# Kernel optimization log

Measured on AMD Instinct MI355X. Metric: run time of the kernel, lower is better.

## Reference

```python
import jax, jax.numpy as jnp
import numpy as np

B, S, D, E, H = 4, 2048, 1024, 8, 2048


def setup_inputs() -> dict:
    key = jax.random.key(0)
    ks = jax.random.split(key, 8)
    s_in = 1.0 / np.sqrt(D)   # torch Linear default init scale (uniform bound)
    s_hid = 1.0 / np.sqrt(H)
    return {
        "x": jax.random.normal(ks[0], (B, S, D), dtype=jnp.float32),
        "W1": jax.random.uniform(ks[1], (E, D, H), minval=-s_in, maxval=s_in, dtype=jnp.float32),
        "b1": jax.random.uniform(ks[2], (E, H), minval=-s_in, maxval=s_in, dtype=jnp.float32),
        "W2": jax.random.uniform(ks[3], (E, H, D), minval=-s_hid, maxval=s_hid, dtype=jnp.float32),
        "b2": jax.random.uniform(ks[4], (E, D), minval=-s_hid, maxval=s_hid, dtype=jnp.float32),
        "Wg": jax.random.uniform(ks[5], (D, E), minval=-s_in, maxval=s_in, dtype=jnp.float32),
        "bg": jax.random.uniform(ks[6], (E,), minval=-s_in, maxval=s_in, dtype=jnp.float32),
    }


def reference(x, W1, b1, W2, b2, Wg, bg):
    # All-experts dense MoE (eval mode: dropout is identity).
    # hidden: [B,S,E,H]
    h = jax.nn.relu(jnp.einsum("bsd,edh->bseh", x, W1) + b1)
    # expert outputs: [B,S,E,D]
    expert_out = jnp.einsum("bseh,ehd->bsed", h, W2) + b2
    # gate (raw linear, no softmax in original): [B,S,E]
    gate = jnp.einsum("bsd,de->bse", x, Wg) + bg
    # gate-weighted sum over experts -> [B,S,D]
    return jnp.einsum("bse,bsed->bsd", gate, expert_out)
```

## Files before the change

### kernel.cpp

```cpp
#include <hip/hip_runtime.h>

#define NTOK 8192
#define DDIM 1024
#define HDIM 2048
#define NEXP 8
#define GEXP 2

#define BM 256
#define BN 128
#define BK 64

typedef unsigned short u16;
typedef short bf16x8 __attribute__((ext_vector_type(8)));
typedef float f32x4 __attribute__((ext_vector_type(4)));
typedef float float4_t __attribute__((ext_vector_type(4)));

__device__ __forceinline__ u16 f2bf(float f) {
  unsigned u = __float_as_uint(f);
  u += 0x7FFFu + ((u >> 16) & 1u);
  return (u16)(u >> 16);
}

#define GLOAD_LDS16(gp, lp)                                                     \
  __builtin_amdgcn_global_load_lds(                                             \
      (const __attribute__((address_space(1))) unsigned int*)(gp),              \
      (__attribute__((address_space(3))) unsigned int*)(lp), 16, 0, 0)

__global__ void k_prep(const float* __restrict__ x, const float* __restrict__ Wg,
                       const float* __restrict__ bg,
                       u16* __restrict__ xb, float* __restrict__ gate) {
  const int tok = (blockIdx.x * 256 + threadIdx.x) >> 6;
  const int lane = threadIdx.x & 63;
  const float* xr = x + (size_t)tok * DDIM;
  u16* xo = xb + (size_t)tok * DDIM;
  float s[NEXP];
#pragma unroll
  for (int e = 0; e < NEXP; ++e) s[e] = 0.f;
#pragma unroll
  for (int it = 0; it < 2; ++it) {
    const int d0 = lane * 8 + it * 512;
    float4_t v0 = *(const float4_t*)(xr + d0);
    float4_t v1 = *(const float4_t*)(xr + d0 + 4);
    union { bf16x8 v; u16 h[8]; } u;
    u.h[0] = f2bf(v0.x); u.h[1] = f2bf(v0.y); u.h[2] = f2bf(v0.z); u.h[3] = f2bf(v0.w);
    u.h[4] = f2bf(v1.x); u.h[5] = f2bf(v1.y); u.h[6] = f2bf(v1.z); u.h[7] = f2bf(v1.w);
    *(bf16x8*)(xo + d0) = u.v;
    float xv[8] = {v0.x, v0.y, v0.z, v0.w, v1.x, v1.y, v1.z, v1.w};
#pragma unroll
    for (int j = 0; j < 8; ++j) {
      const float4_t w0 = *(const float4_t*)(Wg + (size_t)(d0 + j) * NEXP);
      const float4_t w1 = *(const float4_t*)(Wg + (size_t)(d0 + j) * NEXP + 4);
      s[0] += xv[j] * w0.x; s[1] += xv[j] * w0.y;
      s[2] += xv[j] * w0.z; s[3] += xv[j] * w0.w;
      s[4] += xv[j] * w1.x; s[5] += xv[j] * w1.y;
      s[6] += xv[j] * w1.z; s[7] += xv[j] * w1.w;
    }
  }
#pragma unroll
  for (int off = 32; off; off >>= 1)
#pragma unroll
    for (int e = 0; e < NEXP; ++e) s[e] += __shfl_down(s[e], off);
  if (lane == 0) {
#pragma unroll
    for (int e = 0; e < NEXP; ++e) gate[(size_t)tok * NEXP + e] = s[e] + bg[e];
  }
}

__global__ void k_transpose(const float* __restrict__ in, u16* __restrict__ out,
                            int R, int C, size_t oexp, int orstride) {
  __shared__ float t[64][65];
  const int rb = blockIdx.x * 64, cb = blockIdx.y * 64;
  const float* pin = in + (size_t)blockIdx.z * R * C;
  u16* pout = out + (size_t)blockIdx.z * oexp;
  const int tid = threadIdx.x;
  {
    const int r = tid >> 4;
    const int c4 = (tid & 15) * 4;
#pragma unroll
    for (int i = 0; i < 4; ++i) {
      float4_t v = *(const float4_t*)(pin + (size_t)(rb + r + 16 * i) * C + cb + c4);
      t[r + 16 * i][c4 + 0] = v.x;
      t[r + 16 * i][c4 + 1] = v.y;
      t[r + 16 * i][c4 + 2] = v.z;
      t[r + 16 * i][c4 + 3] = v.w;
    }
  }
  __syncthreads();
  {
    const int oc = tid >> 3;
    const int r8 = (tid & 7) * 8;
#pragma unroll
    for (int jp = 0; jp < 2; ++jp) {
      const int ocol = oc + 32 * jp;
      union { bf16x8 v; u16 h[8]; } u;
#pragma unroll
      for (int k = 0; k < 8; ++k) u.h[k] = f2bf(t[r8 + k][ocol]);
      *(bf16x8*)(pout + (size_t)(cb + ocol) * orstride + rb + r8) = u.v;
    }
  }
}

template <int MODE, int BCH>
__global__ __launch_bounds__(512, 2) void k_gemm(
    const u16* __restrict__ A, int lda,
    const u16* __restrict__ Bt, int ldb,
    const float* __restrict__ bias,
    const float* __restrict__ gate, int ebase,
    void* __restrict__ Cout, int ldc,
    int tilesN, int K, int accum) {
  __shared__ __align__(16) u16 lds[3 * (BM + BN) * BK];
  const int tid = threadIdx.x;
  const int lane = tid & 63;
  const int wid = tid >> 6;
  const int wm = wid >> 1;
  const int wn = wid & 1;

  int nwg = gridDim.x, wg = blockIdx.x;
  int q = nwg >> 3, r8 = nwg & 7;
  int xcd = wg & 7, lo = wg >> 3;
  int swz = (xcd < r8 ? xcd * (q + 1) : r8 * (q + 1) + (xcd - r8) * q) + lo;
  int tm = swz / tilesN, tn = swz % tilesN;
  int bm = tm * BM, bn = tn * BN;

  const int srow = tid >> 3;
  const int scol = ((tid & 7) ^ (srow & 7)) << 3;
  const u16* gA = A + (size_t)(bm + srow) * lda + scol;
  const u16* gB = Bt + (size_t)(bn + srow) * ldb + scol;
  const int dofs = wid * 512;

  u16* a0 = lds;            u16* b0 = lds + BM * BK;
  u16* a1 = b0 + BN * BK;   u16* b1p = a1 + BM * BK;
  u16* a2 = b1p + BN * BK;  u16* b2p = a2 + BM * BK;

#define BOFF(kt) (BCH ? ((size_t)((kt) >> 5) * ((size_t)DDIM * HDIM) +          \
                         (size_t)((kt) & 31) * BK)                              \
                      : (size_t)(kt) * BK)

#define STAGE(aD, bD, kt)                                                       \
  {                                                                             \
    const u16* sa_ = gA + (size_t)(kt) * BK;                                    \
    const u16* sb_ = gB + BOFF(kt);                                             \
    GLOAD_LDS16(sa_,                       (aD) + dofs);                        \
    GLOAD_LDS16(sa_ + (size_t)64 * lda,    (aD) + 4096 + dofs);                 \
    GLOAD_LDS16(sa_ + (size_t)128 * lda,   (aD) + 8192 + dofs);                 \
    GLOAD_LDS16(sa_ + (size_t)192 * lda,   (aD) + 12288 + dofs);                \
    GLOAD_LDS16(sb_,                       (bD) + dofs);                        \
    GLOAD_LDS16(sb_ + (size_t)64 * ldb,    (bD) + 4096 + dofs);                 \
  }

  const int fr = lane & 15;
  const int fq = lane >> 4;
  const int xr = fr & 7;
  const int so0 = ((0 + fq) ^ xr) << 3;
  const int so1 = ((4 + fq) ^ xr) << 3;
  int aro[4], bro[4];
#pragma unroll
  for (int m = 0; m < 4; ++m) aro[m] = (wm * 64 + m * 16 + fr) << 6;
#pragma unroll
  for (int n = 0; n < 4; ++n) bro[n] = (wn * 64 + n * 16 + fr) << 6;

  f32x4 acc[4][4] = {};
  const int nkt = K >> 6;

  STAGE(a0, b0, 0);
  STAGE(a1, b1p, 1);
  asm volatile("s_waitcnt vmcnt(6)" ::: "memory");
  __builtin_amdgcn_s_barrier();
  __builtin_amdgcn_sched_barrier(0);

  u16 *aC = a0, *bC = b0, *aN = a1, *bN = b1p, *aF = a2, *bF = b2p;

#pragma unroll 1
  for (int t = 0; t < nkt; ++t) {
    if (t + 2 < nkt) STAGE(aF, bF, t + 2);
#pragma unroll
    for (int kk = 0; kk < 2; ++kk) {
      const int so = kk ? so1 : so0;
      bf16x8 af[4], bfv[4];
#pragma unroll
      for (int m = 0; m < 4; ++m) af[m] = *(const bf16x8*)(aC + aro[m] + so);
#pragma unroll
      for (int n = 0; n < 4; ++n) bfv[n] = *(const bf16x8*)(bC + bro[n] + so);
      __builtin_amdgcn_s_setprio(1);
#pragma unroll
      for (int m = 0; m < 4; ++m)
#pragma unroll
        for (int n = 0; n < 4; ++n)
          acc[m][n] = __builtin_amdgcn_mfma_f32_16x16x32_bf16(af[m], bfv[n],
                                                              acc[m][n], 0, 0, 0);
      __builtin_amdgcn_s_setprio(0);
    }
    if (t != nkt - 1) {
      if (t + 2 < nkt) {
        asm volatile("s_waitcnt vmcnt(6)" ::: "memory");
      } else {
        asm volatile("s_waitcnt vmcnt(0)" ::: "memory");
      }
      __builtin_amdgcn_s_barrier();
      __builtin_amdgcn_sched_barrier(0);
      u16* tp;
      tp = aC; aC = aN; aN = aF; aF = tp;
      tp = bC; bC = bN; bN = bF; bF = tp;
    }
  }

  const int colbase = bn + wn * 64 + fr;
  if (MODE == 1) {
    const int e = ebase + ((bn + wn * 64) >> 11);
    float bcol[4];
#pragma unroll
    for (int n = 0; n < 4; ++n) bcol[n] = bias[colbase + n * 16];
    u16* O = (u16*)Cout;
#pragma unroll
    for (int m = 0; m < 4; ++m) {
#pragma unroll
      for (int j = 0; j < 4; ++j) {
        int r = bm + wm * 64 + m * 16 + fq * 4 + j;
        float g = gate[(size_t)r * NEXP + e];
#pragma unroll
        for (int n = 0; n < 4; ++n) {
          float v = fmaxf(acc[m][n][j] + bcol[n], 0.f) * g;
          O[(size_t)r * ldc + colbase + n * 16] = f2bf(v);
        }
      }
    }
  } else {
    float* O = (float*)Cout;
    float b2c[4][NEXP];
    if (!accum) {
#pragma unroll
      for (int n = 0; n < 4; ++n)
#pragma unroll
        for (int e = 0; e < NEXP; ++e)
          b2c[n][e] = bias[(size_t)e * DDIM + colbase + n * 16];
    }
#pragma unroll
    for (int m = 0; m < 4; ++m) {
#pragma unroll
      for (int j = 0; j < 4; ++j) {
        int r = bm + wm * 64 + m * 16 + fq * 4 + j;
        if (!accum) {
          float g8[NEXP];
#pragma unroll
          for (int e = 0; e < NEXP; ++e) g8[e] = gate[(size_t)r * NEXP + e];
#pragma unroll
          for (int n = 0; n < 4; ++n) {
            float v = acc[m][n][j];
#pragma unroll
            for (int e = 0; e < NEXP; ++e) v += g8[e] * b2c[n][e];
            O[(size_t)r * DDIM + colbase + n * 16] = v;
          }
        } else {
#pragma unroll
          for (int n = 0; n < 4; ++n) {
            size_t idx = (size_t)r * DDIM + colbase + n * 16;
            O[idx] += acc[m][n][j];
          }
        }
      }
    }
  }
#undef STAGE
#undef BOFF
}

extern "C" void kernel_launch(void* const* d_in, const int* in_sizes, int n_in,
                              void* d_out, int out_size, void* d_ws, size_t ws_size,
                              hipStream_t stream) {
  (void)in_sizes; (void)n_in; (void)out_size;
  const float* x  = (const float*)d_in[0];
  const float* W1 = (const float*)d_in[1];
  const float* b1 = (const float*)d_in[2];
  const float* W2 = (const float*)d_in[3];
  const float* b2 = (const float*)d_in[4];
  const float* Wg = (const float*)d_in[5];
  const float* bg = (const float*)d_in[6];
  float* out = (float*)d_out;

  size_t o_xb   = 0;
  size_t o_w1t  = o_xb  + (size_t)NTOK * DDIM * 2;
  size_t o_w2t  = o_w1t + (size_t)NEXP * HDIM * DDIM * 2;
  size_t o_gate = o_w2t + (size_t)NEXP * DDIM * HDIM * 2;
  size_t o_h    = o_gate + (size_t)NTOK * NEXP * 4;
  size_t need   = o_h   + (size_t)NTOK * GEXP * HDIM * 2;
  if (ws_size < need) return;

  u16*   xb   = (u16*)((char*)d_ws + o_xb);
  u16*   W1t  = (u16*)((char*)d_ws + o_w1t);
  u16*   W2t  = (u16*)((char*)d_ws + o_w2t);
  float* gate = (float*)((char*)d_ws + o_gate);
  u16*   hbuf = (u16*)((char*)d_ws + o_h);

  k_prep<<<NTOK / 4, 256, 0, stream>>>(x, Wg, bg, xb, gate);
  dim3 g1(DDIM / 64, HDIM / 64, NEXP);
  k_transpose<<<g1, 256, 0, stream>>>(W1, W1t, DDIM, HDIM, (size_t)HDIM * DDIM, DDIM);
  dim3 g2(HDIM / 64, DDIM / 64, NEXP);
  k_transpose<<<g2, 256, 0, stream>>>(W2, W2t, HDIM, DDIM, (size_t)DDIM * HDIM, HDIM);

  const int Ng = GEXP * HDIM;
  for (int g = 0; g < NEXP / GEXP; ++g) {
    k_gemm<1, 0><<<(NTOK / BM) * (Ng / BN), 512, 0, stream>>>(
        xb, DDIM, W1t + (size_t)g * Ng * DDIM, DDIM,
        b1 + (size_t)g * Ng, gate, g * GEXP,
        hbuf, Ng, Ng / BN, DDIM, 0);
    k_gemm<2, 1><<<(NTOK / BM) * (DDIM / BN), 512, 0, stream>>>(
        hbuf, Ng, W2t + (size_t)g * GEXP * DDIM * HDIM, HDIM,
        b2, gate, 0,
        out, DDIM, DDIM / BN, Ng, g > 0);
  }
}
```

Before: 705.5 us.

## Template GEMM tile shapes, add XCD-grouped tile mapping, restructure K-loop barrier

The GEMM kernel becomes templated on tile shape. The second GEMM now uses 128x256 tiles instead of 256x128, and workgroups are mapped to output tiles in XCD-local rectangular groups to improve L2 reuse of A and B panels. The K-loop is reordered so a single wait-and-barrier runs at the top of each iteration, before the next stage is issued. All LDS fragments for both k-halves are loaded before the MFMAs. This aims to cut redundant global traffic and synchronisation stalls, at the cost of more live registers and fixed hard-coded grid grouping parameters.

```diff
diff --git a/kernel.cpp b/kernel.cpp
--- a/kernel.cpp
+++ b/kernel.cpp
@@ -5,10 +5,6 @@
 #define HDIM 2048
 #define NEXP 8
 #define GEXP 2
-
-#define BM 256
-#define BN 128
-#define BK 64
 
 typedef unsigned short u16;
 typedef short bf16x8 __attribute__((ext_vector_type(8)));
@@ -100,27 +96,26 @@
   }
 }
 
-template <int MODE, int BCH>
+template <int TM, int TN, int MODE, int BCH>
 __global__ __launch_bounds__(512, 2) void k_gemm(
     const u16* __restrict__ A, int lda,
     const u16* __restrict__ Bt, int ldb,
     const float* __restrict__ bias,
     const float* __restrict__ gate, int ebase,
     void* __restrict__ Cout, int ldc,
-    int tilesN, int K, int accum) {
-  __shared__ __align__(16) u16 lds[3 * (BM + BN) * BK];
-  const int tid = threadIdx.x;
-  const int lane = tid & 63;
-  const int wid = tid >> 6;
-  const int wm = wid >> 1;
-  const int wn = wid & 1;
-
-  int nwg = gridDim.x, wg = blockIdx.x;
-  int q = nwg >> 3, r8 = nwg & 7;
-  int xcd = wg & 7, lo = wg >> 3;
-  int swz = (xcd < r8 ? xcd * (q + 1) : r8 * (q + 1) + (xcd - r8) * q) + lo;
-  int tm = swz / tilesN, tn = swz % tilesN;
-  int bm = tm * BM, bn = tn * BN;
+    int K, int accum, int ca, int cb, int cgcols) {
+  constexpr int WN = TN / 64;
+  constexpr int BUFE = (TM + TN) * 64;
+  __shared__ __align__(16) u16 lds[3 * BUFE];
+  const int tid = threadIdx.x, lane = tid & 63, wid = tid >> 6;
+  const int wm = wid / WN, wn = wid % WN;
+
+  const int wg = blockIdx.x;
+  const int xcd = wg & 7, lo = wg >> 3;
+  const int cr = xcd / cgcols, cc = xcd % cgcols;
+  const int tm = cr * ca + lo / cb;
+  const int tn = cc * cb + lo % cb;
+  const int bm = tm * TM, bn = tn * TN;
 
   const int srow = tid >> 3;
   const int scol = ((tid & 7) ^ (srow & 7)) << 3;
@@ -128,99 +123,84 @@
   const u16* gB = Bt + (size_t)(bn + srow) * ldb + scol;
   const int dofs = wid * 512;
 
-  u16* a0 = lds;            u16* b0 = lds + BM * BK;
-  u16* a1 = b0 + BN * BK;   u16* b1p = a1 + BM * BK;
-  u16* a2 = b1p + BN * BK;  u16* b2p = a2 + BM * BK;
+  u16* buf0 = lds;
+  u16* buf1 = lds + BUFE;
+  u16* buf2 = lds + 2 * BUFE;
 
 #define BOFF(kt) (BCH ? ((size_t)((kt) >> 5) * ((size_t)DDIM * HDIM) +          \
-                         (size_t)((kt) & 31) * BK)                              \
-                      : (size_t)(kt) * BK)
-
-#define STAGE(aD, bD, kt)                                                       \
-  {                                                                             \
-    const u16* sa_ = gA + (size_t)(kt) * BK;                                    \
-    const u16* sb_ = gB + BOFF(kt);                                             \
-    GLOAD_LDS16(sa_,                       (aD) + dofs);                        \
-    GLOAD_LDS16(sa_ + (size_t)64 * lda,    (aD) + 4096 + dofs);                 \
-    GLOAD_LDS16(sa_ + (size_t)128 * lda,   (aD) + 8192 + dofs);                 \
-    GLOAD_LDS16(sa_ + (size_t)192 * lda,   (aD) + 12288 + dofs);                \
-    GLOAD_LDS16(sb_,                       (bD) + dofs);                        \
-    GLOAD_LDS16(sb_ + (size_t)64 * ldb,    (bD) + 4096 + dofs);                 \
-  }
-
-  const int fr = lane & 15;
-  const int fq = lane >> 4;
-  const int xr = fr & 7;
+                         (size_t)((kt) & 31) * 64)                              \
+                      : (size_t)(kt) * 64)
+#define STAGE(dst, kt)                                                          \
+  { _Pragma("unroll") for (int c_ = 0; c_ < TM / 64; ++c_)                      \
+      GLOAD_LDS16(gA + (size_t)(c_ * 64) * lda + (size_t)(kt) * 64,             \
+                  (dst) + c_ * 4096 + dofs);                                    \
+    _Pragma("unroll") for (int c_ = 0; c_ < TN / 64; ++c_)                      \
+      GLOAD_LDS16(gB + (size_t)(c_ * 64) * ldb + BOFF(kt),                      \
+                  (dst) + (TM / 64 + c_) * 4096 + dofs); }
+
+  const int fr = lane & 15, fq = lane >> 4, xr = fr & 7;
   const int so0 = ((0 + fq) ^ xr) << 3;
   const int so1 = ((4 + fq) ^ xr) << 3;
-  int aro[4], bro[4];
-#pragma unroll
-  for (int m = 0; m < 4; ++m) aro[m] = (wm * 64 + m * 16 + fr) << 6;
-#pragma unroll
-  for (int n = 0; n < 4; ++n) bro[n] = (wn * 64 + n * 16 + fr) << 6;
 
   f32x4 acc[4][4] = {};
   const int nkt = K >> 6;
 
-  STAGE(a0, b0, 0);
-  STAGE(a1, b1p, 1);
-  asm volatile("s_waitcnt vmcnt(6)" ::: "memory");
-  __builtin_amdgcn_s_barrier();
-  __builtin_amdgcn_sched_barrier(0);
-
-  u16 *aC = a0, *bC = b0, *aN = a1, *bN = b1p, *aF = a2, *bF = b2p;
+  STAGE(buf0, 0);
+  STAGE(buf1, 1);
+  u16 *bC = buf0, *bN = buf1, *bF = buf2;
 
 #pragma unroll 1
   for (int t = 0; t < nkt; ++t) {
-    if (t + 2 < nkt) STAGE(aF, bF, t + 2);
-#pragma unroll
-    for (int kk = 0; kk < 2; ++kk) {
-      const int so = kk ? so1 : so0;
-      bf16x8 af[4], bfv[4];
-#pragma unroll
-      for (int m = 0; m < 4; ++m) af[m] = *(const bf16x8*)(aC + aro[m] + so);
-#pragma unroll
-      for (int n = 0; n < 4; ++n) bfv[n] = *(const bf16x8*)(bC + bro[n] + so);
-      __builtin_amdgcn_s_setprio(1);
-#pragma unroll
-      for (int m = 0; m < 4; ++m)
-#pragma unroll
-        for (int n = 0; n < 4; ++n)
-          acc[m][n] = __builtin_amdgcn_mfma_f32_16x16x32_bf16(af[m], bfv[n],
-                                                              acc[m][n], 0, 0, 0);
-      __builtin_amdgcn_s_setprio(0);
-    }
-    if (t != nkt - 1) {
-      if (t + 2 < nkt) {
-        asm volatile("s_waitcnt vmcnt(6)" ::: "memory");
-      } else {
-        asm volatile("s_waitcnt vmcnt(0)" ::: "memory");
+    if (t + 1 < nkt) { asm volatile("s_waitcnt vmcnt(6)" ::: "memory"); }
+    else             { asm volatile("s_waitcnt vmcnt(0)" ::: "memory"); }
+    __builtin_amdgcn_s_barrier();
+    __builtin_amdgcn_sched_barrier(0);
+    if (t + 2 < nkt) STAGE(bF, t + 2);
+    const u16* aP = bC;
+    const u16* bP = bC + TM * 64;
+    bf16x8 av[4][2], bv[4][2];
+#pragma unroll
+    for (int mi = 0; mi < 4; ++mi) {
+      const int rb_ = (wm * 64 + mi * 16 + fr) << 6;
+      av[mi][0] = *(const bf16x8*)(aP + rb_ + so0);
+      av[mi][1] = *(const bf16x8*)(aP + rb_ + so1);
+    }
+#pragma unroll
+    for (int ni = 0; ni < 4; ++ni) {
+      const int rb_ = (wn * 64 + ni * 16 + fr) << 6;
+      bv[ni][0] = *(const bf16x8*)(bP + rb_ + so0);
+      bv[ni][1] = *(const bf16x8*)(bP + rb_ + so1);
+    }
+    __builtin_amdgcn_s_setprio(1);
+#pragma unroll
+    for (int mi = 0; mi < 4; ++mi)
+#pragma unroll
+      for (int ni = 0; ni < 4; ++ni) {
+        acc[mi][ni] = __builtin_amdgcn_mfma_f32_16x16x32_bf16(
+            av[mi][0], bv[ni][0], acc[mi][ni], 0, 0, 0);
+        acc[mi][ni] = __builtin_amdgcn_mfma_f32_16x16x32_bf16(
+            av[mi][1], bv[ni][1], acc[mi][ni], 0, 0, 0);
       }
-      __builtin_amdgcn_s_barrier();
-      __builtin_amdgcn_sched_barrier(0);
-      u16* tp;
-      tp = aC; aC = aN; aN = aF; aF = tp;
-      tp = bC; bC = bN; bN = bF; bF = tp;
-    }
-  }
-
-  const int colbase = bn + wn * 64 + fr;
+    __builtin_amdgcn_s_setprio(0);
+    u16* tp = bC; bC = bN; bN = bF; bF = tp;
+  }
+
   if (MODE == 1) {
-    const int e = ebase + ((bn + wn * 64) >> 11);
+    u16* O = (u16*)Cout;
+    const int e = ebase + (bn >> 11);
     float bcol[4];
 #pragma unroll
-    for (int n = 0; n < 4; ++n) bcol[n] = bias[colbase + n * 16];
-    u16* O = (u16*)Cout;
-#pragma unroll
-    for (int m = 0; m < 4; ++m) {
+    for (int ni = 0; ni < 4; ++ni) bcol[ni] = bias[bn + wn * 64 + ni * 16 + fr];
+#pragma unroll
+    for (int mi = 0; mi < 4; ++mi) {
 #pragma unroll
       for (int j = 0; j < 4; ++j) {
-        int r = bm + wm * 64 + m * 16 + fq * 4 + j;
-        float g = gate[(size_t)r * NEXP + e];
-#pragma unroll
-        for (int n = 0; n < 4; ++n) {
-          float v = fmaxf(acc[m][n][j] + bcol[n], 0.f) * g;
-          O[(size_t)r * ldc + colbase + n * 16] = f2bf(v);
+        const int r = bm + wm * 64 + mi * 16 + fq * 4 + j;
+        const float g = gate[(size_t)r * NEXP + e];
+#pragma unroll
+        for (int ni = 0; ni < 4; ++ni) {
+          float v = fmaxf(acc[mi][ni][j] + bcol[ni], 0.f) * g;
+          O[(size_t)r * ldc + bn + wn * 64 + ni * 16 + fr] = f2bf(v);
         }
       }
     }
@@ -229,32 +209,32 @@
     float b2c[4][NEXP];
     if (!accum) {
 #pragma unroll
-      for (int n = 0; n < 4; ++n)
+      for (int ni = 0; ni < 4; ++ni)
 #pragma unroll
         for (int e = 0; e < NEXP; ++e)
-          b2c[n][e] = bias[(size_t)e * DDIM + colbase + n * 16];
-    }
-#pragma unroll
-    for (int m = 0; m < 4; ++m) {
+          b2c[ni][e] = bias[(size_t)e * DDIM + bn + wn * 64 + ni * 16 + fr];
+    }
+#pragma unroll
+    for (int mi = 0; mi < 4; ++mi) {
 #pragma unroll
       for (int j = 0; j < 4; ++j) {
-        int r = bm + wm * 64 + m * 16 + fq * 4 + j;
+        const int r = bm + wm * 64 + mi * 16 + fq * 4 + j;
         if (!accum) {
           float g8[NEXP];
 #pragma unroll
           for (int e = 0; e < NEXP; ++e) g8[e] = gate[(size_t)r * NEXP + e];
 #pragma unroll
-          for (int n = 0; n < 4; ++n) {
-            float v = acc[m][n][j];
-#pragma unroll
-            for (int e = 0; e < NEXP; ++e) v += g8[e] * b2c[n][e];
-            O[(size_t)r * DDIM + colbase + n * 16] = v;
+          for (int ni = 0; ni < 4; ++ni) {
+            float v = acc[mi][ni][j];
+#pragma unroll
+            for (int e = 0; e < NEXP; ++e) v += g8[e] * b2c[ni][e];
+            O[(size_t)r * DDIM + bn + wn * 64 + ni * 16 + fr] = v;
           }
         } else {
 #pragma unroll
-          for (int n = 0; n < 4; ++n) {
-            size_t idx = (size_t)r * DDIM + colbase + n * 16;
-            O[idx] += acc[m][n][j];
+          for (int ni = 0; ni < 4; ++ni) {
+            const size_t idx = (size_t)r * DDIM + bn + wn * 64 + ni * 16 + fr;
+            O[idx] += acc[mi][ni][j];
           }
         }
       }
@@ -299,13 +279,13 @@
 
   const int Ng = GEXP * HDIM;
   for (int g = 0; g < NEXP / GEXP; ++g) {
-    k_gemm<1, 0><<<(NTOK / BM) * (Ng / BN), 512, 0, stream>>>(
+    k_gemm<256, 128, 1, 0><<<1024, 512, 0, stream>>>(
         xb, DDIM, W1t + (size_t)g * Ng * DDIM, DDIM,
         b1 + (size_t)g * Ng, gate, g * GEXP,
-        hbuf, Ng, Ng / BN, DDIM, 0);
-    k_gemm<2, 1><<<(NTOK / BM) * (DDIM / BN), 512, 0, stream>>>(
+        hbuf, Ng, DDIM, 0, 16, 8, 4);
+    k_gemm<128, 256, 2, 1><<<256, 512, 0, stream>>>(
         hbuf, Ng, W2t + (size_t)g * GEXP * DDIM * HDIM, HDIM,
         b2, gate, 0,
-        out, DDIM, DDIM / BN, Ng, g > 0);
-  }
-}
+        out, DDIM, Ng, g > 0, 8, 4, 1);
+  }
+}
```

After: 683.7 us. 3.1% less time.
